# Optimization experiments

Measured on AMD Instinct MI355X. Metric: run time of the kernel, lower is better.

## Reference

```python
import jax, jax.numpy as jnp
import numpy as np

B, T, EMB, HEAD = 8, 2048, 1024, 1024

def setup_inputs() -> dict:
    key = jax.random.key(0)
    k1, k2, k3, k4 = jax.random.split(key, 4)
    s = 1.0 / np.sqrt(EMB)
    return {
        "x": jax.random.normal(k1, (B, T, EMB), dtype=jnp.float32),
        "Wq": jax.random.normal(k2, (HEAD, EMB), dtype=jnp.float32) * s,
        "Wk": jax.random.normal(k3, (HEAD, EMB), dtype=jnp.float32) * s,
        "Wv": jax.random.normal(k4, (HEAD, EMB), dtype=jnp.float32) * s,
    }

def reference(x, Wq, Wk, Wv):
    # Bias-free projections; torch Linear weight is [out, in] -> contract on last dim.
    q = jnp.einsum('btc,hc->bth', x, Wq)  # [B,T,HEAD]
    k = jnp.einsum('btc,hc->bth', x, Wk)
    v = jnp.einsum('btc,hc->bth', x, Wv)
    C = x.shape[-1]
    scale = jnp.asarray(C, x.dtype) ** -0.5  # NOTE: scales by emb dim C, as in source
    wei = jnp.einsum('bth,bsh->bts', q, k) * scale  # [B,T,T]
    Tn = x.shape[1]
    causal = jnp.tril(jnp.ones((Tn, Tn), dtype=bool))
    wei = jnp.where(causal, wei, -jnp.inf)
    wei = jax.nn.softmax(wei, axis=-1)
    # dropout omitted (eval mode / deterministic reference)
    out = jnp.einsum('bts,bsh->bth', wei, v)  # [B,T,HEAD]
    return out
```

## Files before the change

### kernel.cpp

```cpp
#include <hip/hip_runtime.h>

typedef unsigned short u16;
typedef short short8 __attribute__((ext_vector_type(8)));
typedef float f32x4 __attribute__((ext_vector_type(4)));

#define WS_K_OFF    33554432ULL
#define WS_PTRI     67108864ULL
#define WS_PART     104857600ULL
#define WS_RINV     105381888ULL
#define WS_NEED     105447424ULL

__device__ __forceinline__ u16 f2bf(float f) {
    union { float f; unsigned u; } c; c.f = f;
    unsigned r = c.u + 0x7fffu + ((c.u >> 16) & 1u);
    return (u16)(r >> 16);
}
__device__ __forceinline__ float bf2f(u16 h) {
    union { unsigned u; float f; } c; c.u = ((unsigned)h) << 16; return c.f;
}
__device__ __forceinline__ void gll16(const u16* g, u16* l) {
    __builtin_amdgcn_global_load_lds(
        (const __attribute__((address_space(1))) void*)g,
        (__attribute__((address_space(3))) void*)l, 16, 0, 0);
}

template<int AMODE>
__device__ __forceinline__ void gemm_pipe(
    const u16* __restrict__ A, int lda,
    const u16* __restrict__ B, int ldb,
    int m0, int n0, int nk, u16* lds, f32x4 acc[8][4])
{
    const int tid  = threadIdx.x;
    const int lane = tid & 63;
    const int w    = tid >> 6;
    const int wm   = w >> 2, wn = w & 3;
    const int kg   = lane >> 4, l15 = lane & 15;
    const int r0   = w * 32 + (lane >> 2);
    const int s0   = (lane & 3) ^ ((r0 >> 1) & 3);

    const int ldA = AMODE ? 256 : lda;
    const u16* Ar0 = A + (size_t)(m0 + r0) * ldA + s0 * 8;
    const u16* Ar1 = Ar0 + 16 * ldA;
    const u16* Br0 = B + (size_t)(n0 + r0) * ldb + s0 * 8;
    const u16* Br1 = Br0 + 16 * ldb;

    auto aoff = [&](int t) -> int {
        return AMODE ? ((t >> 3) * 65536 + (t & 7) * 32) : t * 32;
    };
    auto STAGE = [&](int t) {
        const int ao = aoff(t), bo = t * 32, buf = (t & 3) * 16384;
        u16* dA = lds + buf + w * 1024;
        u16* dB = lds + buf + 8192 + w * 1024;
        gll16(Ar0 + ao, dA);
        gll16(Ar1 + ao, dA + 512);
        gll16(Br0 + bo, dB);
        gll16(Br1 + bo, dB + 512);
    };
    auto LDA8 = [&](short8* fa, int t) {
        const u16* h = lds + (t & 3) * 16384 + wm * 128 * 32;
        #pragma unroll
        for (int mt = 0; mt < 8; ++mt) {
            const int row = mt * 16 + l15;
            fa[mt] = *reinterpret_cast<const short8*>(
                h + row * 32 + ((kg ^ ((row >> 1) & 3)) << 3));
        }
    };
    auto LDB4 = [&](short8* fb, int t) {
        const u16* h = lds + (t & 3) * 16384 + 8192 + wn * 64 * 32;
        #pragma unroll
        for (int nt = 0; nt < 4; ++nt) {
            const int row = nt * 16 + l15;
            fb[nt] = *reinterpret_cast<const short8*>(
                h + row * 32 + ((kg ^ ((row >> 1) & 3)) << 3));
        }
    };
    auto MFMA32 = [&](short8* fa, short8* fb) {
        __builtin_amdgcn_s_setprio(1);
        #pragma unroll
        for (int mt = 0; mt < 8; ++mt)
            #pragma unroll
            for (int nt = 0; nt < 4; ++nt)
                acc[mt][nt] = __builtin_amdgcn_mfma_f32_16x16x32_bf16(
                    fa[mt], fb[nt], acc[mt][nt], 0, 0, 0);
        __builtin_amdgcn_s_setprio(0);
    };

    STAGE(0); STAGE(1); STAGE(2);
    asm volatile("s_waitcnt vmcnt(4)" ::: "memory");
    __builtin_amdgcn_s_barrier();

    short8 faA[8], faB[8], fb[4];
    LDA8(faA, 0);

    for (int t = 0; t < nk; t += 2) {
        LDB4(fb, t);
        LDA8(faB, t + 1);
        if (t + 3 < nk) STAGE(t + 3);
        MFMA32(faA, fb);
        if (t + 3 < nk) asm volatile("s_waitcnt vmcnt(4)" ::: "memory");
        else            asm volatile("s_waitcnt vmcnt(0)" ::: "memory");
        __builtin_amdgcn_s_barrier();

        LDB4(fb, t + 1);
        if (t + 2 < nk) LDA8(faA, t + 2);
        if (t + 4 < nk) STAGE(t + 4);
        MFMA32(faB, fb);
        if (t + 4 < nk) asm volatile("s_waitcnt vmcnt(4)" ::: "memory");
        else            asm volatile("s_waitcnt vmcnt(0)" ::: "memory");
        __builtin_amdgcn_s_barrier();
    }
}

__global__ __launch_bounds__(256) void cvt_bf16(
    const float* __restrict__ x,
    const float* __restrict__ Wq,
    const float* __restrict__ Wk,
    const float* __restrict__ Wv,
    u16* __restrict__ dst)
{
    const size_t e = ((size_t)blockIdx.x * 256 + threadIdx.x) * 8;
    const float* src;
    if (e < (size_t)16777216) {
        src = x + e;
    } else {
        size_t j = e - 16777216;
        int z = (int)(j >> 20);
        const float* Wz = (z == 0) ? Wq : (z == 1) ? Wk : Wv;
        src = Wz + (j & 1048575);
    }
    float4 a = *reinterpret_cast<const float4*>(src);
    float4 b = *reinterpret_cast<const float4*>(src + 4);
    short8 v;
    v[0] = (short)f2bf(a.x); v[1] = (short)f2bf(a.y);
    v[2] = (short)f2bf(a.z); v[3] = (short)f2bf(a.w);
    v[4] = (short)f2bf(b.x); v[5] = (short)f2bf(b.y);
    v[6] = (short)f2bf(b.z); v[7] = (short)f2bf(b.w);
    *reinterpret_cast<short8*>(dst + e) = v;
}

__global__ __launch_bounds__(512, 2) void qkv_pipe(
    const u16* __restrict__ xb, const u16* __restrict__ Wb,
    u16* __restrict__ Qo, u16* __restrict__ Ko, u16* __restrict__ VTo, int zbase)
{
    __shared__ u16 L[65536];
    const int tid = threadIdx.x, lane = tid & 63, w = tid >> 6;
    const int wm = w >> 2, wn = w & 3, kg = lane >> 4, l15 = lane & 15;
    const int m0 = blockIdx.x * 256, n0 = blockIdx.y * 256;
    const int z = blockIdx.z + zbase;

    const f32x4 z4 = {0.f, 0.f, 0.f, 0.f};
    f32x4 acc[8][4];
    #pragma unroll
    for (int i = 0; i < 8; ++i)
        #pragma unroll
        for (int j = 0; j < 4; ++j) acc[i][j] = z4;

    gemm_pipe<0>(xb, 1024, Wb + (size_t)z * 1048576, 1024, m0, n0, 32, L, acc);

    if (z < 2) {
        u16* O = (z == 0) ? Qo : Ko;
        #pragma unroll
        for (int mt = 0; mt < 8; ++mt) {
            const int row0 = m0 + wm * 128 + mt * 16 + kg * 4;
            #pragma unroll
            for (int nt = 0; nt < 4; ++nt) {
                const int col = n0 + wn * 64 + nt * 16 + l15;
                #pragma unroll
                for (int r = 0; r < 4; ++r)
                    O[(size_t)(row0 + r) * 1024 + col] = f2bf(acc[mt][nt][r]);
            }
        }
    } else {
        #pragma unroll
        for (int mt = 0; mt < 8; ++mt) {
            const int row0 = m0 + wm * 128 + mt * 16 + kg * 4;
            #pragma unroll
            for (int nt = 0; nt < 4; ++nt) {
                const int col = n0 + wn * 64 + nt * 16 + l15;
                #pragma unroll
                for (int r = 0; r < 4; ++r) {
                    const int rr = row0 + r;
                    VTo[((size_t)(rr >> 11) * 1024 + col) * 2048 + (rr & 2047)] = f2bf(acc[mt][nt][r]);
                }
            }
        }
    }
}

__global__ __launch_bounds__(512, 2) void sp_new(
    const u16* __restrict__ Q, const u16* __restrict__ K,
    u16* __restrict__ Ptri, float* __restrict__ partials)
{
    const int qb = blockIdx.x, kb = blockIdx.y, b = blockIdx.z;
    if (kb > qb) return;
    __shared__ u16 L[65536];
    const int tid = threadIdx.x, lane = tid & 63, w = tid >> 6;
    const int wm = w >> 2, wn = w & 3, kg = lane >> 4, l15 = lane & 15;

    const f32x4 z4 = {0.f, 0.f, 0.f, 0.f};
    f32x4 acc[8][4];
    #pragma unroll
    for (int i = 0; i < 8; ++i)
        #pragma unroll
        for (int j = 0; j < 4; ++j) acc[i][j] = z4;

    gemm_pipe<0>(Q, 1024, K, 1024, b * 2048 + qb * 256, b * 2048 + kb * 256, 32, L, acc);

    u16* Pt = Ptri + ((size_t)b * 36 + (qb * (qb + 1)) / 2 + kb) * 65536;
    float* psum = (float*)L;
    #pragma unroll
    for (int mt = 0; mt < 8; ++mt) {
        const int lt0 = wm * 128 + mt * 16 + kg * 4;
        #pragma unroll
        for (int r = 0; r < 4; ++r) {
            const int lt = lt0 + r;
            const int gt = qb * 256 + lt;
            float ps = 0.f;
            #pragma unroll
            for (int nt = 0; nt < 4; ++nt) {
                const int lcol = wn * 64 + nt * 16 + l15;
                const int gs = kb * 256 + lcol;
                const float p = (gs <= gt) ? __expf(acc[mt][nt][r] * 0.03125f) : 0.f;
                ps += p;
                Pt[(size_t)lt * 256 + lcol] = f2bf(p);
            }
            #pragma unroll
            for (int d = 1; d < 16; d <<= 1) ps += __shfl_xor(ps, d, 64);
            if (l15 == 0) psum[lt * 4 + wn] = ps;
        }
    }
    __syncthreads();
    if (tid < 256) {
        const float s = psum[tid * 4] + psum[tid * 4 + 1] + psum[tid * 4 + 2] + psum[tid * 4 + 3];
        partials[((size_t)b * 2048 + qb * 256 + tid) * 8 + kb] = s;
    }
}

__global__ __launch_bounds__(512, 2) void sp_old(
    const u16* __restrict__ Q, const u16* __restrict__ K, u16* __restrict__ P)
{
    const int qb = blockIdx.x, kb = blockIdx.y, b = blockIdx.z;
    if (kb > qb) return;
    __shared__ u16 L[65536];
    const int tid = threadIdx.x, lane = tid & 63, w = tid >> 6;
    const int wm = w >> 2, wn = w & 3, kg = lane >> 4, l15 = lane & 15;

    const f32x4 z4 = {0.f, 0.f, 0.f, 0.f};
    f32x4 acc[8][4];
    #pragma unroll
    for (int i = 0; i < 8; ++i)
        #pragma unroll
        for (int j = 0; j < 4; ++j) acc[i][j] = z4;

    gemm_pipe<0>(Q, 1024, K, 1024, b * 2048 + qb * 256, b * 2048 + kb * 256, 32, L, acc);

    u16* Pb = P + (size_t)b * 2048 * 2048;
    #pragma unroll
    for (int mt = 0; mt < 8; ++mt) {
        const int trow0 = qb * 256 + wm * 128 + mt * 16 + kg * 4;
        #pragma unroll
        for (int nt = 0; nt < 4; ++nt) {
            const int scol = kb * 256 + wn * 64 + nt * 16 + l15;
            #pragma unroll
            for (int r = 0; r < 4; ++r) {
                const int trow = trow0 + r;
                const float p = (scol <= trow) ? __expf(acc[mt][nt][r] * 0.03125f) : 0.f;
                Pb[(size_t)trow * 2048 + scol] = f2bf(p);
            }
        }
    }
}

__global__ __launch_bounds__(256) void rowsum_k(
    const float* __restrict__ partials, float* __restrict__ rinv)
{
    const int row = blockIdx.x * 256 + threadIdx.x;
    const int qb = (row & 2047) >> 8;
    float s = 0.f;
    for (int kb = 0; kb <= qb; ++kb) s += partials[(size_t)row * 8 + kb];
    rinv[row] = 1.f / s;
}

__global__ __launch_bounds__(512, 2) void pv_new(
    const u16* __restrict__ Ptri, const u16* __restrict__ VT,
    const float* __restrict__ rinv, float* __restrict__ out)
{
    const int b = blockIdx.x >> 3, qblk = blockIdx.x & 7;
    const int nb = blockIdx.y;
    const int nk = (qblk + 1) * 8;
    __shared__ u16 L[65536];
    const int tid = threadIdx.x, lane = tid & 63, w = tid >> 6;
    const int wm = w >> 2, wn = w & 3, kg = lane >> 4, l15 = lane & 15;

    const f32x4 z4 = {0.f, 0.f, 0.f, 0.f};
    f32x4 acc[8][4];
    #pragma unroll
    for (int i = 0; i < 8; ++i)
        #pragma unroll
        for (int j = 0; j < 4; ++j) acc[i][j] = z4;

    const u16* Aq = Ptri + ((size_t)b * 36 + (qblk * (qblk + 1)) / 2) * 65536;
    gemm_pipe<1>(Aq, 256, VT + (size_t)b * 1024 * 2048, 2048, 0, nb * 256, nk, L, acc);

    #pragma unroll
    for (int mt = 0; mt < 8; ++mt) {
        const int lt0 = wm * 128 + mt * 16 + kg * 4;
        const int grow0 = b * 2048 + qblk * 256 + lt0;
        float rs[4];
        #pragma unroll
        for (int r = 0; r < 4; ++r) rs[r] = rinv[grow0 + r];
        #pragma unroll
        for (int nt = 0; nt < 4; ++nt) {
            const int col = nb * 256 + wn * 64 + nt * 16 + l15;
            #pragma unroll
            for (int r = 0; r < 4; ++r)
                out[(size_t)(grow0 + r) * 1024 + col] = acc[mt][nt][r] * rs[r];
        }
    }
}

__global__ __launch_bounds__(512, 2) void pv_old(
    const u16* __restrict__ P, const u16* __restrict__ VT, float* __restrict__ Of)
{
    const int b = blockIdx.x >> 3, qblk = blockIdx.x & 7;
    const int nb = blockIdx.y;
    const int nk = (qblk + 1) * 8;
    __shared__ u16 L[65536];
    const int tid = threadIdx.x, lane = tid & 63, w = tid >> 6;
    const int wm = w >> 2, wn = w & 3, kg = lane >> 4, l15 = lane & 15;

    const f32x4 z4 = {0.f, 0.f, 0.f, 0.f};
    f32x4 acc[8][4];
    #pragma unroll
    for (int i = 0; i < 8; ++i)
        #pragma unroll
        for (int j = 0; j < 4; ++j) acc[i][j] = z4;

    gemm_pipe<0>(P + (size_t)b * 2048 * 2048, 2048,
                 VT + (size_t)b * 1024 * 2048, 2048,
                 qblk * 256, nb * 256, nk, L, acc);

    #pragma unroll
    for (int mt = 0; mt < 8; ++mt) {
        const int trow0 = qblk * 256 + wm * 128 + mt * 16 + kg * 4;
        #pragma unroll
        for (int nt = 0; nt < 4; ++nt) {
            const int col = nb * 256 + wn * 64 + nt * 16 + l15;
            #pragma unroll
            for (int r = 0; r < 4; ++r)
                Of[((size_t)b * 2048 + trow0 + r) * 1024 + col] = acc[mt][nt][r];
        }
    }
}

__global__ __launch_bounds__(256) void finalize(
    const u16* __restrict__ P, const float* __restrict__ Of, float* __restrict__ out)
{
    const int row = blockIdx.x;
    const int tid = threadIdx.x;
    const int b = row >> 11, t = row & 2047;
    const int len = ((t >> 8) + 1) * 256;
    const u16* prow = P + ((size_t)b * 2048 + t) * 2048;

    float s = 0.f;
    const int i = tid * 8;
    if (i < len) {
        short8 v = *reinterpret_cast<const short8*>(prow + i);
        #pragma unroll
        for (int j = 0; j < 8; ++j) s += bf2f((u16)v[j]);
    }
    #pragma unroll
    for (int d = 1; d < 64; d <<= 1) s += __shfl_xor(s, d, 64);

    __shared__ float red[4];
    if ((tid & 63) == 0) red[tid >> 6] = s;
    __syncthreads();
    const float rinv = 1.f / (red[0] + red[1] + red[2] + red[3]);

    const size_t o = (size_t)row * 1024 + tid * 4;
    f32x4 v = *reinterpret_cast<const f32x4*>(Of + o);
    v[0] *= rinv; v[1] *= rinv; v[2] *= rinv; v[3] *= rinv;
    *reinterpret_cast<f32x4*>(out + o) = v;
}

extern "C" void kernel_launch(void* const* d_in, const int* in_sizes, int n_in,
                              void* d_out, int out_size, void* d_ws, size_t ws_size,
                              hipStream_t stream) {
    const float* x  = (const float*)d_in[0];
    const float* Wq = (const float*)d_in[1];
    const float* Wk = (const float*)d_in[2];
    const float* Wv = (const float*)d_in[3];

    u16* xb = (u16*)d_out;
    u16* Wb = xb + (size_t)16777216;

    cvt_bf16<<<dim3(9728), 256, 0, stream>>>(x, Wq, Wk, Wv, xb);

    if (ws_size >= WS_NEED) {
        u16*   Qb   = (u16*)d_ws;
        u16*   Kb   = (u16*)((char*)d_ws + WS_K_OFF);
        u16*   Pt   = (u16*)((char*)d_ws + WS_PTRI);
        float* part = (float*)((char*)d_ws + WS_PART);
        float* rinv = (float*)((char*)d_ws + WS_RINV);
        u16*   VTb  = Qb;

        qkv_pipe<<<dim3(64, 4, 2), 512, 0, stream>>>(xb, Wb, Qb, Kb, Qb, 0);
        sp_new<<<dim3(8, 8, 8), 512, 0, stream>>>(Qb, Kb, Pt, part);
        rowsum_k<<<dim3(64), 256, 0, stream>>>(part, rinv);
        qkv_pipe<<<dim3(64, 4, 1), 512, 0, stream>>>(xb, Wb, Qb, Kb, VTb, 2);
        pv_new<<<dim3(64, 4), 512, 0, stream>>>(Pt, VTb, rinv, (float*)d_out);
    } else {
        u16* Qb  = (u16*)d_ws;
        u16* Kb  = Qb + (size_t)16384 * 1024;
        u16* VTb = Kb + (size_t)16384 * 1024;
        float* Of = (float*)d_ws;
        u16* Pb = (u16*)d_out;

        qkv_pipe<<<dim3(64, 4, 3), 512, 0, stream>>>(xb, Wb, Qb, Kb, VTb, 0);
        sp_old<<<dim3(8, 8, 8), 512, 0, stream>>>(Qb, Kb, Pb);
        pv_old<<<dim3(64, 4), 512, 0, stream>>>(Pb, VTb, Of);
        finalize<<<dim3(16384), 256, 0, stream>>>(Pb, Of, (float*)d_out);
    }
}
```

Before: 267.2 us.

## Split GEMM k-step into two half-tile MFMA phases with separate A/B staging

Restructures the GEMM main loop: each k-step now loads half of the A fragments, issues 16 MFMAs, then loads the other half and issues 16 more, with the A and B global-to-LDS loads split across the two phases. This drops the double-buffered register fragments (faA/faB), which lowers VGPR pressure, and interleaves barriers so memory traffic overlaps compute in a finer pattern. The cost is more barriers per k-step and explicit lgkmcnt waits right before the MFMAs, so LDS read latency is less hidden than with the previous register prefetch.

After: 279.3 us. +4.5%, slower.

```diff
diff --git a/kernel.cpp b/kernel.cpp
--- a/kernel.cpp
+++ b/kernel.cpp
@@ -47,26 +47,27 @@
     auto aoff = [&](int t) -> int {
         return AMODE ? ((t >> 3) * 65536 + (t & 7) * 32) : t * 32;
     };
-    auto STAGE = [&](int t) {
-        const int ao = aoff(t), bo = t * 32, buf = (t & 3) * 16384;
-        u16* dA = lds + buf + w * 1024;
-        u16* dB = lds + buf + 8192 + w * 1024;
-        gll16(Ar0 + ao, dA);
-        gll16(Ar1 + ao, dA + 512);
-        gll16(Br0 + bo, dB);
-        gll16(Br1 + bo, dB + 512);
+    auto STAGE_A = [&](int t) {
+        u16* dA = lds + (t & 3) * 16384 + w * 1024;
+        gll16(Ar0 + aoff(t), dA);
+        gll16(Ar1 + aoff(t), dA + 512);
     };
-    auto LDA8 = [&](short8* fa, int t) {
-        const u16* h = lds + (t & 3) * 16384 + wm * 128 * 32;
-        #pragma unroll
-        for (int mt = 0; mt < 8; ++mt) {
-            const int row = mt * 16 + l15;
-            fa[mt] = *reinterpret_cast<const short8*>(
+    auto STAGE_B = [&](int t) {
+        u16* dB = lds + (t & 3) * 16384 + 8192 + w * 1024;
+        gll16(Br0 + t * 32, dB);
+        gll16(Br1 + t * 32, dB + 512);
+    };
+    auto LDA4 = [&](short8* fa, int t, int mb) {
+        const u16* h = lds + (t & 3) * 16384 + wm * 4096;
+        #pragma unroll
+        for (int mi = 0; mi < 4; ++mi) {
+            const int row = (mb + mi) * 16 + l15;
+            fa[mi] = *reinterpret_cast<const short8*>(
                 h + row * 32 + ((kg ^ ((row >> 1) & 3)) << 3));
         }
     };
     auto LDB4 = [&](short8* fb, int t) {
-        const u16* h = lds + (t & 3) * 16384 + 8192 + wn * 64 * 32;
+        const u16* h = lds + (t & 3) * 16384 + 8192 + wn * 2048;
         #pragma unroll
         for (int nt = 0; nt < 4; ++nt) {
             const int row = nt * 16 + l15;
@@ -74,39 +75,50 @@
                 h + row * 32 + ((kg ^ ((row >> 1) & 3)) << 3));
         }
     };
-    auto MFMA32 = [&](short8* fa, short8* fb) {
+
+    STAGE_A(0); STAGE_B(0);
+    STAGE_A(1); STAGE_B(1);
+    STAGE_A(2); STAGE_B(2);
+    asm volatile("s_waitcnt vmcnt(8)" ::: "memory");
+    __builtin_amdgcn_s_barrier();
+
+    short8 fa[4], fb[4];
+    for (int t = 0; t < nk; ++t) {
+        LDB4(fb, t);
+        LDA4(fa, t, 0);
+        if (t + 3 < nk) STAGE_A(t + 3);
+        __builtin_amdgcn_s_barrier();
+        asm volatile("s_waitcnt lgkmcnt(0)" ::: "memory");
+        __builtin_amdgcn_sched_barrier(0);
         __builtin_amdgcn_s_setprio(1);
         #pragma unroll
-        for (int mt = 0; mt < 8; ++mt)
+        for (int mi = 0; mi < 4; ++mi)
             #pragma unroll
             for (int nt = 0; nt < 4; ++nt)
-                acc[mt][nt] = __builtin_amdgcn_mfma_f32_16x16x32_bf16(
-                    fa[mt], fb[nt], acc[mt][nt], 0, 0, 0);
+                acc[mi][nt] = __builtin_amdgcn_mfma_f32_16x16x32_bf16(
+                    fa[mi], fb[nt], acc[mi][nt], 0, 0, 0);
         __builtin_amdgcn_s_setprio(0);
-    };
-
-    STAGE(0); STAGE(1); STAGE(2);
-    asm volatile("s_waitcnt vmcnt(4)" ::: "memory");
-    __builtin_amdgcn_s_barrier();
-
-    short8 faA[8], faB[8], fb[4];
-    LDA8(faA, 0);
-
-    for (int t = 0; t < nk; t += 2) {
-        LDB4(fb, t);
-        LDA8(faB, t + 1);
-        if (t + 3 < nk) STAGE(t + 3);
-        MFMA32(faA, fb);
-        if (t + 3 < nk) asm volatile("s_waitcnt vmcnt(4)" ::: "memory");
-        else            asm volatile("s_waitcnt vmcnt(0)" ::: "memory");
         __builtin_amdgcn_s_barrier();
 
-        LDB4(fb, t + 1);
-        if (t + 2 < nk) LDA8(faA, t + 2);
-        if (t + 4 < nk) STAGE(t + 4);
-        MFMA32(faB, fb);
-        if (t + 4 < nk) asm volatile("s_waitcnt vmcnt(4)" ::: "memory");
-        else            asm volatile("s_waitcnt vmcnt(0)" ::: "memory");
+        LDA4(fa, t, 4);
+        if (t + 3 < nk) STAGE_B(t + 3);
+        __builtin_amdgcn_s_barrier();
+        asm volatile("s_waitcnt lgkmcnt(0)" ::: "memory");
+        __builtin_amdgcn_sched_barrier(0);
+        __builtin_amdgcn_s_setprio(1);
+        #pragma unroll
+        for (int mi = 0; mi < 4; ++mi)
+            #pragma unroll
+            for (int nt = 0; nt < 4; ++nt)
+                acc[4 + mi][nt] = __builtin_amdgcn_mfma_f32_16x16x32_bf16(
+                    fa[mi], fb[nt], acc[4 + mi][nt], 0, 0, 0);
+        __builtin_amdgcn_s_setprio(0);
+        {
+            const int rem = nk - 2 - t;
+            if (rem >= 2)      asm volatile("s_waitcnt vmcnt(8)" ::: "memory");
+            else if (rem == 1) asm volatile("s_waitcnt vmcnt(4)" ::: "memory");
+            else               asm volatile("s_waitcnt vmcnt(0)" ::: "memory");
+        }
         __builtin_amdgcn_s_barrier();
     }
 }
```

## Fuse Q/K projections sharing x tiles, fold rowsum into a 128-wide PV kernel

Applied to the files above, without the earlier changes.

The Q and K projections become one kernel that stages each x tile once and runs MFMAs against both weight tiles, with a 3-stage LDS ring and two accumulator sets at occupancy 1. The separate rowsum kernel is removed: the PV kernel now sums the softmax partials itself and keeps the reciprocal in LDS. PV switches to 256x128 output tiles over 512 blocks ordered heaviest-causal-block first, to improve load balance and SM fill. The risks are high register pressure in the fused QK kernel (64 accumulators per thread) and extra V traffic from the narrower PV tiles.

After: 600.9 us. 125% more time.

```diff
diff --git a/kernel.cpp b/kernel.cpp
--- a/kernel.cpp
+++ b/kernel.cpp
@@ -7,7 +7,6 @@
 #define WS_K_OFF    33554432ULL
 #define WS_PTRI     67108864ULL
 #define WS_PART     104857600ULL
-#define WS_RINV     105381888ULL
 #define WS_NEED     105447424ULL
 
 __device__ __forceinline__ u16 f2bf(float f) {
@@ -57,7 +56,7 @@
         gll16(Br1 + bo, dB + 512);
     };
     auto LDA8 = [&](short8* fa, int t) {
-        const u16* h = lds + (t & 3) * 16384 + wm * 128 * 32;
+        const u16* h = lds + (t & 3) * 16384 + wm * 4096;
         #pragma unroll
         for (int mt = 0; mt < 8; ++mt) {
             const int row = mt * 16 + l15;
@@ -66,7 +65,7 @@
         }
     };
     auto LDB4 = [&](short8* fb, int t) {
-        const u16* h = lds + (t & 3) * 16384 + 8192 + wn * 64 * 32;
+        const u16* h = lds + (t & 3) * 16384 + 8192 + wn * 2048;
         #pragma unroll
         for (int nt = 0; nt < 4; ++nt) {
             const int row = nt * 16 + l15;
@@ -74,7 +73,7 @@
                 h + row * 32 + ((kg ^ ((row >> 1) & 3)) << 3));
         }
     };
-    auto MFMA32 = [&](short8* fa, short8* fb) {
+    auto MFMA32 = [&](short8* fa, short8* fb, int mb) {
         __builtin_amdgcn_s_setprio(1);
         #pragma unroll
         for (int mt = 0; mt < 8; ++mt)
@@ -83,6 +82,7 @@
                 acc[mt][nt] = __builtin_amdgcn_mfma_f32_16x16x32_bf16(
                     fa[mt], fb[nt], acc[mt][nt], 0, 0, 0);
         __builtin_amdgcn_s_setprio(0);
+        (void)mb;
     };
 
     STAGE(0); STAGE(1); STAGE(2);
@@ -96,7 +96,7 @@
         LDB4(fb, t);
         LDA8(faB, t + 1);
         if (t + 3 < nk) STAGE(t + 3);
-        MFMA32(faA, fb);
+        MFMA32(faA, fb, 0);
         if (t + 3 < nk) asm volatile("s_waitcnt vmcnt(4)" ::: "memory");
         else            asm volatile("s_waitcnt vmcnt(0)" ::: "memory");
         __builtin_amdgcn_s_barrier();
@@ -104,7 +104,7 @@
         LDB4(fb, t + 1);
         if (t + 2 < nk) LDA8(faA, t + 2);
         if (t + 4 < nk) STAGE(t + 4);
-        MFMA32(faB, fb);
+        MFMA32(faB, fb, 0);
         if (t + 4 < nk) asm volatile("s_waitcnt vmcnt(4)" ::: "memory");
         else            asm volatile("s_waitcnt vmcnt(0)" ::: "memory");
         __builtin_amdgcn_s_barrier();
@@ -138,6 +138,101 @@
     *reinterpret_cast<short8*>(dst + e) = v;
 }
 
+__global__ __launch_bounds__(512, 1) void qk_fused(
+    const u16* __restrict__ xb,
+    const u16* __restrict__ Wb,
+    u16* __restrict__ Qo, u16* __restrict__ Ko)
+{
+    __shared__ u16 L[73728];
+    const int tid = threadIdx.x, lane = tid & 63, w = tid >> 6;
+    const int wm = w >> 2, wn = w & 3, kg = lane >> 4, l15 = lane & 15;
+    const int m0 = blockIdx.x * 256, n0 = blockIdx.y * 256;
+    const int nk = 32;
+
+    const int r0 = w * 32 + (lane >> 2);
+    const int s0 = (lane & 3) ^ ((r0 >> 1) & 3);
+    const u16* Ar0 = xb + (size_t)(m0 + r0) * 1024 + s0 * 8;
+    const u16* Ar1 = Ar0 + 16 * 1024;
+    const u16* Bq0 = Wb + (size_t)(n0 + r0) * 1024 + s0 * 8;
+    const u16* Bq1 = Bq0 + 16 * 1024;
+    const u16* Bk0 = Bq0 + (size_t)1048576;
+    const u16* Bk1 = Bq1 + (size_t)1048576;
+
+    const f32x4 z4 = {0.f, 0.f, 0.f, 0.f};
+    f32x4 accq[8][4], acck[8][4];
+    #pragma unroll
+    for (int i = 0; i < 8; ++i)
+        #pragma unroll
+        for (int j = 0; j < 4; ++j) { accq[i][j] = z4; acck[i][j] = z4; }
+
+    auto STAGE = [&](int t) {
+        const int bo = t * 32;
+        u16* d = L + (t % 3) * 24576 + w * 1024;
+        gll16(Ar0 + bo, d);
+        gll16(Ar1 + bo, d + 512);
+        gll16(Bq0 + bo, d + 8192);
+        gll16(Bq1 + bo, d + 8192 + 512);
+        gll16(Bk0 + bo, d + 16384);
+        gll16(Bk1 + bo, d + 16384 + 512);
+    };
+
+    STAGE(0); STAGE(1);
+    asm volatile("s_waitcnt vmcnt(6)" ::: "memory");
+    __builtin_amdgcn_s_barrier();
+
+    for (int t = 0; t < nk; ++t) {
+        const u16* hb = L + (t % 3) * 24576;
+        short8 fa[8], fbq[4], fbk[4];
+        #pragma unroll
+        for (int mt = 0; mt < 8; ++mt) {
+            const int row = mt * 16 + l15;
+            fa[mt] = *reinterpret_cast<const short8*>(
+                hb + wm * 4096 + row * 32 + ((kg ^ ((row >> 1) & 3)) << 3));
+        }
+        #pragma unroll
+        for (int nt = 0; nt < 4; ++nt) {
+            const int row = nt * 16 + l15;
+            const int off = wn * 2048 + row * 32 + ((kg ^ ((row >> 1) & 3)) << 3);
+            fbq[nt] = *reinterpret_cast<const short8*>(hb + 8192  + off);
+            fbk[nt] = *reinterpret_cast<const short8*>(hb + 16384 + off);
+        }
+        if (t + 2 < nk) STAGE(t + 2);
+
+        __builtin_amdgcn_s_setprio(1);
+        #pragma unroll
+        for (int mt = 0; mt < 8; ++mt)
+            #pragma unroll
+            for (int nt = 0; nt < 4; ++nt)
+                accq[mt][nt] = __builtin_amdgcn_mfma_f32_16x16x32_bf16(
+                    fa[mt], fbq[nt], accq[mt][nt], 0, 0, 0);
+        #pragma unroll
+        for (int mt = 0; mt < 8; ++mt)
+            #pragma unroll
+            for (int nt = 0; nt < 4; ++nt)
+                acck[mt][nt] = __builtin_amdgcn_mfma_f32_16x16x32_bf16(
+                    fa[mt], fbk[nt], acck[mt][nt], 0, 0, 0);
+        __builtin_amdgcn_s_setprio(0);
+
+        if (t + 2 < nk) asm volatile("s_waitcnt vmcnt(6)" ::: "memory");
+        else            asm volatile("s_waitcnt vmcnt(0)" ::: "memory");
+        __builtin_amdgcn_s_barrier();
+    }
+
+    #pragma unroll
+    for (int mt = 0; mt < 8; ++mt) {
+        const int row0 = m0 + wm * 128 + mt * 16 + kg * 4;
+        #pragma unroll
+        for (int nt = 0; nt < 4; ++nt) {
+            const int col = n0 + wn * 64 + nt * 16 + l15;
+            #pragma unroll
+            for (int r = 0; r < 4; ++r) {
+                Qo[(size_t)(row0 + r) * 1024 + col] = f2bf(accq[mt][nt][r]);
+                Ko[(size_t)(row0 + r) * 1024 + col] = f2bf(acck[mt][nt][r]);
+            }
+        }
+    }
+}
+
 __global__ __launch_bounds__(512, 2) void qkv_pipe(
     const u16* __restrict__ xb, const u16* __restrict__ Wb,
     u16* __restrict__ Qo, u16* __restrict__ Ko, u16* __restrict__ VTo, int zbase)
@@ -271,50 +366,123 @@
     }
 }
 
-__global__ __launch_bounds__(256) void rowsum_k(
-    const float* __restrict__ partials, float* __restrict__ rinv)
-{
-    const int row = blockIdx.x * 256 + threadIdx.x;
-    const int qb = (row & 2047) >> 8;
-    float s = 0.f;
-    for (int kb = 0; kb <= qb; ++kb) s += partials[(size_t)row * 8 + kb];
-    rinv[row] = 1.f / s;
-}
-
-__global__ __launch_bounds__(512, 2) void pv_new(
+__global__ __launch_bounds__(512, 2) void pv128(
     const u16* __restrict__ Ptri, const u16* __restrict__ VT,
-    const float* __restrict__ rinv, float* __restrict__ out)
-{
-    const int b = blockIdx.x >> 3, qblk = blockIdx.x & 7;
-    const int nb = blockIdx.y;
-    const int nk = (qblk + 1) * 8;
-    __shared__ u16 L[65536];
+    const float* __restrict__ part, float* __restrict__ out)
+{
+    __shared__ u16 L[49152];
+    const int i = blockIdx.x;
+    const int q  = 7 - (i >> 6);
+    const int b  = (i >> 3) & 7;
+    const int nb = i & 7;
+    const int nk = (q + 1) * 8;
+
     const int tid = threadIdx.x, lane = tid & 63, w = tid >> 6;
-    const int wm = w >> 2, wn = w & 3, kg = lane >> 4, l15 = lane & 15;
+    const int wm = w >> 1, wn = w & 1, kg = lane >> 4, l15 = lane & 15;
+
+    const u16* A = Ptri + ((size_t)b * 36 + (q * (q + 1)) / 2) * 65536;
+    const u16* B = VT + ((size_t)b * 1024 + nb * 128) * 2048;
+
+    const int rA = w * 32 + (lane >> 2);
+    const int sA = (lane & 3) ^ ((rA >> 1) & 3);
+    const int rB = w * 16 + (lane >> 2);
+    const int sB = (lane & 3) ^ ((rB >> 1) & 3);
+    const u16* Ar0 = A + (size_t)rA * 256 + sA * 8;
+    const u16* Ar1 = Ar0 + 16 * 256;
+    const u16* Br0 = B + (size_t)rB * 2048 + sB * 8;
 
     const f32x4 z4 = {0.f, 0.f, 0.f, 0.f};
-    f32x4 acc[8][4];
-    #pragma unroll
-    for (int i = 0; i < 8; ++i)
-        #pragma unroll
-        for (int j = 0; j < 4; ++j) acc[i][j] = z4;
-
-    const u16* Aq = Ptri + ((size_t)b * 36 + (qblk * (qblk + 1)) / 2) * 65536;
-    gemm_pipe<1>(Aq, 256, VT + (size_t)b * 1024 * 2048, 2048, 0, nb * 256, nk, L, acc);
-
-    #pragma unroll
-    for (int mt = 0; mt < 8; ++mt) {
-        const int lt0 = wm * 128 + mt * 16 + kg * 4;
-        const int grow0 = b * 2048 + qblk * 256 + lt0;
+    f32x4 acc[4][4];
+    #pragma unroll
+    for (int a_ = 0; a_ < 4; ++a_)
+        #pragma unroll
+        for (int j = 0; j < 4; ++j) acc[a_][j] = z4;
+
+    auto aoff = [&](int t) -> int { return (t >> 3) * 65536 + (t & 7) * 32; };
+    auto STAGE = [&](int t) {
+        const int buf = (t & 3) * 12288;
+        u16* dA = L + buf + w * 1024;
+        u16* dB = L + buf + 8192 + w * 512;
+        gll16(Ar0 + aoff(t), dA);
+        gll16(Ar1 + aoff(t), dA + 512);
+        gll16(Br0 + t * 32, dB);
+    };
+    auto LDA4 = [&](short8* fa, int t) {
+        const u16* h = L + (t & 3) * 12288;
+        #pragma unroll
+        for (int mt = 0; mt < 4; ++mt) {
+            const int row = wm * 64 + mt * 16 + l15;
+            fa[mt] = *reinterpret_cast<const short8*>(
+                h + row * 32 + ((kg ^ ((row >> 1) & 3)) << 3));
+        }
+    };
+    auto LDB4 = [&](short8* fb, int t) {
+        const u16* h = L + (t & 3) * 12288 + 8192;
+        #pragma unroll
+        for (int nt = 0; nt < 4; ++nt) {
+            const int row = wn * 64 + nt * 16 + l15;
+            fb[nt] = *reinterpret_cast<const short8*>(
+                h + row * 32 + ((kg ^ ((row >> 1) & 3)) << 3));
+        }
+    };
+    auto MFMA16 = [&](short8* fa, short8* fb) {
+        __builtin_amdgcn_s_setprio(1);
+        #pragma unroll
+        for (int mt = 0; mt < 4; ++mt)
+            #pragma unroll
+            for (int nt = 0; nt < 4; ++nt)
+                acc[mt][nt] = __builtin_amdgcn_mfma_f32_16x16x32_bf16(
+                    fa[mt], fb[nt], acc[mt][nt], 0, 0, 0);
+        __builtin_amdgcn_s_setprio(0);
+    };
+
+    STAGE(0); STAGE(1); STAGE(2);
+    asm volatile("s_waitcnt vmcnt(3)" ::: "memory");
+    __builtin_amdgcn_s_barrier();
+
+    short8 faA[4], faB[4], fb[4];
+    LDA4(faA, 0);
+
+    for (int t = 0; t < nk; t += 2) {
+        LDB4(fb, t);
+        LDA4(faB, t + 1);
+        if (t + 3 < nk) STAGE(t + 3);
+        MFMA16(faA, fb);
+        if (t + 3 < nk) asm volatile("s_waitcnt vmcnt(3)" ::: "memory");
+        else            asm volatile("s_waitcnt vmcnt(0)" ::: "memory");
+        __builtin_amdgcn_s_barrier();
+
+        LDB4(fb, t + 1);
+        if (t + 2 < nk) LDA4(faA, t + 2);
+        if (t + 4 < nk) STAGE(t + 4);
+        MFMA16(faB, fb);
+        if (t + 4 < nk) asm volatile("s_waitcnt vmcnt(3)" ::: "memory");
+        else            asm volatile("s_waitcnt vmcnt(0)" ::: "memory");
+        __builtin_amdgcn_s_barrier();
+    }
+
+    float* Lf = (float*)L;
+    if (tid < 256) {
+        const size_t grow = (size_t)b * 2048 + q * 256 + tid;
+        float s = 0.f;
+        for (int kb = 0; kb <= q; ++kb) s += part[grow * 8 + kb];
+        Lf[tid] = 1.f / s;
+    }
+    __syncthreads();
+
+    #pragma unroll
+    for (int mt = 0; mt < 4; ++mt) {
+        const int lt0 = wm * 64 + mt * 16 + kg * 4;
+        const size_t grow0 = (size_t)b * 2048 + q * 256 + lt0;
         float rs[4];
         #pragma unroll
-        for (int r = 0; r < 4; ++r) rs[r] = rinv[grow0 + r];
-        #pragma unroll
-        for (int nt = 0; nt < 4; ++nt) {
-            const int col = nb * 256 + wn * 64 + nt * 16 + l15;
+        for (int r = 0; r < 4; ++r) rs[r] = Lf[lt0 + r];
+        #pragma unroll
+        for (int nt = 0; nt < 4; ++nt) {
+            const int col = nb * 128 + wn * 64 + nt * 16 + l15;
             #pragma unroll
             for (int r = 0; r < 4; ++r)
-                out[(size_t)(grow0 + r) * 1024 + col] = acc[mt][nt][r] * rs[r];
+                out[(grow0 + r) * 1024 + col] = acc[mt][nt][r] * rs[r];
         }
     }
 }
@@ -401,14 +569,12 @@
         u16*   Kb   = (u16*)((char*)d_ws + WS_K_OFF);
         u16*   Pt   = (u16*)((char*)d_ws + WS_PTRI);
         float* part = (float*)((char*)d_ws + WS_PART);
-        float* rinv = (float*)((char*)d_ws + WS_RINV);
         u16*   VTb  = Qb;
 
-        qkv_pipe<<<dim3(64, 4, 2), 512, 0, stream>>>(xb, Wb, Qb, Kb, Qb, 0);
+        qk_fused<<<dim3(64, 4), 512, 0, stream>>>(xb, Wb, Qb, Kb);
         sp_new<<<dim3(8, 8, 8), 512, 0, stream>>>(Qb, Kb, Pt, part);
-        rowsum_k<<<dim3(64), 256, 0, stream>>>(part, rinv);
         qkv_pipe<<<dim3(64, 4, 1), 512, 0, stream>>>(xb, Wb, Qb, Kb, VTb, 2);
-        pv_new<<<dim3(64, 4), 512, 0, stream>>>(Pt, VTb, rinv, (float*)d_out);
+        pv128<<<dim3(512), 512, 0, stream>>>(Pt, VTb, part, (float*)d_out);
     } else {
         u16* Qb  = (u16*)d_ws;
         u16* Kb  = Qb + (size_t)16384 * 1024;
```
